# Optimization experiments

Measured on AMD Instinct MI355X. Metric: run time of the kernel, lower is better.

## Reference

```python
import jax, jax.numpy as jnp
import numpy as np

NUM_HEADS = 16
THETA = 10000.0

def _apply_rope(x, positions):
    # x: [B, H, S, dh] with interleaved pairs; positions: [B, S] int
    dh = x.shape[-1]
    inv_freq = THETA ** (-jnp.arange(0, dh, 2, dtype=jnp.float32) / dh)  # [dh/2]
    ang = positions.astype(jnp.float32)[:, None, :, None] * inv_freq  # [B,1,S,dh/2]
    cos, sin = jnp.cos(ang), jnp.sin(ang)
    x1, x2 = x[..., 0::2], x[..., 1::2]
    out_even = x1 * cos - x2 * sin
    out_odd = x1 * sin + x2 * cos
    return jnp.stack([out_even, out_odd], axis=-1).reshape(x.shape)

def setup_inputs() -> dict:
    B, S, D = 2, 2048, 2048
    key = jax.random.key(0)
    ks = jax.random.split(key, 5)
    scale = 0.02
    inp = {
        'in_features': jax.random.normal(ks[0], (B, S, D), dtype=jnp.float32),
        'token_positions': jnp.broadcast_to(jnp.arange(S, dtype=jnp.int32), (B, S)),
        'mask': jnp.tril(jnp.ones((S, S), dtype=bool)),
        'q_proj_weight': jax.random.normal(ks[1], (D, D), dtype=jnp.float32) * scale,
        'k_proj_weight': jax.random.normal(ks[2], (D, D), dtype=jnp.float32) * scale,
        'v_proj_weight': jax.random.normal(ks[3], (D, D), dtype=jnp.float32) * scale,
        'o_proj_weight': jax.random.normal(ks[4], (D, D), dtype=jnp.float32) * scale,
    }
    return inp

def reference(in_features, token_positions, mask, q_proj_weight, k_proj_weight, v_proj_weight, o_proj_weight):
    B, S, d_in = in_features.shape
    d_k = q_proj_weight.shape[0]
    d_v = v_proj_weight.shape[0]
    H = NUM_HEADS
    dk_head, dv_head = d_k // H, d_v // H
    Q = jnp.einsum('bsd,kd->bsk', in_features, q_proj_weight).reshape(B, S, H, dk_head).transpose(0, 2, 1, 3)
    K = jnp.einsum('bsd,kd->bsk', in_features, k_proj_weight).reshape(B, S, H, dk_head).transpose(0, 2, 1, 3)
    V = jnp.einsum('bsd,vd->bsv', in_features, v_proj_weight).reshape(B, S, H, dv_head).transpose(0, 2, 1, 3)
    Q = _apply_rope(Q, token_positions)
    K = _apply_rope(K, token_positions)
    scores = jnp.einsum('bhqd,bhkd->bhqk', Q, K) / jnp.sqrt(jnp.float32(dk_head))
    scores = jnp.where(mask[None, None, :, :], scores, jnp.finfo(scores.dtype).min)
    attn = jax.nn.softmax(scores, axis=-1)
    out = jnp.einsum('bhqk,bhkd->bhqd', attn, V)  # [B,H,S,dv_head]
    out = out.transpose(0, 2, 1, 3).reshape(B, S, d_v)
    return jnp.einsum('bsv,mv->bsm', out, o_proj_weight)
```

## Files before the change

kernel.cpp:

```cpp
#include <hip/hip_runtime.h>
#include <hip/hip_bf16.h>
#include <cstdint>

typedef __bf16 bf16_t;
typedef __bf16 bf16x8 __attribute__((ext_vector_type(8)));
typedef __bf16 bf16x4 __attribute__((ext_vector_type(4)));
typedef float  f32x4  __attribute__((ext_vector_type(4)));

#define B_  2
#define S_  2048
#define D_  2048
#define H_  16
#define DH_ 128
#define LDQ 6144

__device__ __forceinline__ void gload_lds16(const bf16_t* g, bf16_t* l) {
    __builtin_amdgcn_global_load_lds(
        (const __attribute__((address_space(1))) void*)g,
        (__attribute__((address_space(3))) void*)l, 16, 0, 0);
}

__global__ __launch_bounds__(256)
void cast_all_k(const float* __restrict__ X,  const float* __restrict__ Wq,
                const float* __restrict__ Wk, const float* __restrict__ Wv,
                const float* __restrict__ Wo,
                bf16_t* __restrict__ Xb, bf16_t* __restrict__ Wqkv,
                bf16_t* __restrict__ Wob) {
    long bid = blockIdx.x;
    const float* src; bf16_t* dst; long off;
    if      (bid <  8192) { src = X;  dst = Xb;             off = bid;         }
    else if (bid < 12288) { src = Wq; dst = Wqkv;           off = bid - 8192;  }
    else if (bid < 16384) { src = Wk; dst = Wqkv + 4194304; off = bid - 12288; }
    else if (bid < 20480) { src = Wv; dst = Wqkv + 8388608; off = bid - 16384; }
    else                  { src = Wo; dst = Wob;            off = bid - 20480; }
    long i = (off * 256 + threadIdx.x) * 4;
    float4 v = *(const float4*)(src + i);
    bf16x4 o = {(bf16_t)v.x, (bf16_t)v.y, (bf16_t)v.z, (bf16_t)v.w};
    *(bf16x4*)(dst + i) = o;
}

template<bool C_BF16>
__global__ __launch_bounds__(256)
void gemm_nt(const bf16_t* __restrict__ A, int lda,
             const bf16_t* __restrict__ B, int ldb,
             void* __restrict__ Cp, int ldc, int K) {
    __shared__ bf16_t As[128 * 32];
    __shared__ bf16_t Bs[128 * 32];
    const int tid  = threadIdx.x;
    const int wave = tid >> 6;
    const int lane = tid & 63;

    const int ntx = gridDim.x;
    const int nwg = ntx * gridDim.y;
    const int lin = blockIdx.y * ntx + blockIdx.x;
    const int swz = (lin & 7) * (nwg >> 3) + (lin >> 3);
    const long bm = (long)(swz / ntx) * 128;
    const long bn = (long)(swz % ntx) * 128;

    const int srow0 = wave * 16 + (lane >> 2);
    const int srow1 = (4 + wave) * 16 + (lane >> 2);
    const int scol  = (lane & 3) * 8;
    const bf16_t* Ag0 = A + (bm + srow0) * (long)lda + scol;
    const bf16_t* Ag1 = A + (bm + srow1) * (long)lda + scol;
    const bf16_t* Bg0 = B + (bn + srow0) * (long)ldb + scol;
    const bf16_t* Bg1 = B + (bn + srow1) * (long)ldb + scol;
    bf16_t* Al0 = &As[wave * 512];
    bf16_t* Al1 = &As[(4 + wave) * 512];
    bf16_t* Bl0 = &Bs[wave * 512];
    bf16_t* Bl1 = &Bs[(4 + wave) * 512];

    const int wr = (wave >> 1) * 64;
    const int wc = (wave & 1) * 64;
    const int fr = lane & 15;
    const int ko = (lane >> 4) * 8;

    f32x4 acc[4][4] = {};

    for (int k0 = 0; k0 < K; k0 += 32) {
        gload_lds16(Ag0 + k0, Al0);
        gload_lds16(Ag1 + k0, Al1);
        gload_lds16(Bg0 + k0, Bl0);
        gload_lds16(Bg1 + k0, Bl1);
        __syncthreads();
        bf16x8 a[4], b[4];
#pragma unroll
        for (int i = 0; i < 4; ++i)
            a[i] = *(const bf16x8*)&As[(wr + i * 16 + fr) * 32 + ko];
#pragma unroll
        for (int j = 0; j < 4; ++j)
            b[j] = *(const bf16x8*)&Bs[(wc + j * 16 + fr) * 32 + ko];
#pragma unroll
        for (int i = 0; i < 4; ++i)
#pragma unroll
            for (int j = 0; j < 4; ++j)
                acc[i][j] = __builtin_amdgcn_mfma_f32_16x16x32_bf16(a[i], b[j], acc[i][j], 0, 0, 0);
        __syncthreads();
    }

#pragma unroll
    for (int i = 0; i < 4; ++i) {
        long r0 = bm + wr + i * 16 + (lane >> 4) * 4;
#pragma unroll
        for (int j = 0; j < 4; ++j) {
            long cc = bn + wc + j * 16 + (lane & 15);
#pragma unroll
            for (int v = 0; v < 4; ++v) {
                if (C_BF16)
                    ((bf16_t*)Cp)[(r0 + v) * (long)ldc + cc] = (bf16_t)acc[i][j][v];
                else
                    ((float*)Cp)[(r0 + v) * (long)ldc + cc] = acc[i][j][v];
            }
        }
    }
}

__global__ __launch_bounds__(256)
void rope_qk_k(bf16_t* __restrict__ QKV, const int* __restrict__ pos) {
    int t = blockIdx.x * 256 + threadIdx.x;
    int g = t & 15;
    int h = (t >> 4) & 15;
    int s = (t >> 8) & 2047;
    int b = t >> 19;
    long qa = ((long)(b * S_ + s)) * LDQ + h * DH_ + g * 8;
    long ka = qa + D_;
    float p = (float)pos[b * S_ + s];
    bf16x8 q = *(bf16x8*)(QKV + qa);
    bf16x8 k = *(bf16x8*)(QKV + ka);
#pragma unroll
    for (int e = 0; e < 4; ++e) {
        int i = g * 4 + e;
        float invf = exp2f(-(float)i * 0.20762050593045702f);
        float ang = p * invf;
        float sn, cs;
        __sincosf(ang, &sn, &cs);
        float q1 = (float)q[2 * e], q2 = (float)q[2 * e + 1];
        q[2 * e]     = (bf16_t)(q1 * cs - q2 * sn);
        q[2 * e + 1] = (bf16_t)(q1 * sn + q2 * cs);
        float k1 = (float)k[2 * e], k2 = (float)k[2 * e + 1];
        k[2 * e]     = (bf16_t)(k1 * cs - k2 * sn);
        k[2 * e + 1] = (bf16_t)(k1 * sn + k2 * cs);
    }
    *(bf16x8*)(QKV + qa) = q;
    *(bf16x8*)(QKV + ka) = k;
}

__global__ __launch_bounds__(256)
void transpose_v_k(const bf16_t* __restrict__ QKV, bf16_t* __restrict__ Vt) {
    __shared__ bf16_t tile[64][80];
    int t = threadIdx.x;
    int bh = blockIdx.z;
    int b = bh >> 4, h = bh & 15;
    long s0 = (long)blockIdx.x * 64;
    int d0 = blockIdx.y * 64;
    const bf16_t* src = QKV + ((long)b * S_ + s0) * LDQ + 2 * D_ + h * DH_ + d0;
#pragma unroll
    for (int p = 0; p < 2; ++p) {
        int r = (t >> 3) + p * 32;
        int c = (t & 7) * 8;
        *(bf16x8*)&tile[r][c] = *(const bf16x8*)&src[(long)r * LDQ + c];
    }
    __syncthreads();
    bf16_t* dst = Vt + ((long)bh * DH_ + d0) * S_ + s0;
#pragma unroll
    for (int p = 0; p < 2; ++p) {
        int d = (t >> 3) + p * 32;
        int c = (t & 7) * 8;
        bf16x8 v;
#pragma unroll
        for (int e = 0; e < 8; ++e) v[e] = tile[c + e][d];
        *(bf16x8*)&dst[(long)d * S_ + c] = v;
    }
}

__device__ __forceinline__ bf16x8 ldsw(const bf16_t* p, int row, int ecol) {
    return *(const bf16x8*)(p + row * 128 + (ecol ^ ((row & 7) << 3)));
}

__global__ __launch_bounds__(512, 1)
void flash_attn_k(const bf16_t* __restrict__ QKV, const bf16_t* __restrict__ Vt,
                  bf16_t* __restrict__ O) {
    __shared__ bf16_t Ksh[2][128 * 128];
    __shared__ bf16_t Vsh[2][128 * 128];
    __shared__ bf16_t Psh[128 * 128];

    const int tid  = threadIdx.x;
    const int w    = tid >> 6;
    const int lane = tid & 63;
    const int fr   = lane & 15;
    const int hi   = lane >> 4;
    const int hi8  = hi * 8;
    const int hi4  = hi * 4;
    const int w16  = w * 16;

    const int bid = blockIdx.x;
    const int qi  = 15 - (bid >> 5);
    const int bh  = bid & 31;
    const int b   = bh >> 4;
    const int h   = bh & 15;
    const long bS   = (long)b * S_;
    const int  qoff = h * DH_;
    const int  koff = D_ + h * DH_;
    const long vbase = (long)bh * DH_;

#pragma unroll
    for (int p = 0; p < 4; ++p) {
        int idx = p * 512 + tid;
        int row = idx >> 4;
        int sl  = (idx & 15) ^ (row & 7);
        gload_lds16(QKV + (bS + qi * 128 + row) * (long)LDQ + qoff + sl * 8,
                    &Psh[(p * 512 + w * 64) * 8]);
    }
#pragma unroll
    for (int p = 0; p < 4; ++p) {
        int idx = p * 512 + tid;
        int row = idx >> 4;
        int sl  = (idx & 15) ^ (row & 7);
        gload_lds16(QKV + (bS + row) * (long)LDQ + koff + sl * 8,
                    &Ksh[0][(p * 512 + w * 64) * 8]);
        gload_lds16(Vt + (vbase + row) * S_ + sl * 8,
                    &Vsh[0][(p * 512 + w * 64) * 8]);
    }
    asm volatile("s_waitcnt vmcnt(8)" ::: "memory");
    __builtin_amdgcn_s_barrier();
    asm volatile("" ::: "memory");

    bf16x8 qfrag[4];
#pragma unroll
    for (int kk = 0; kk < 4; ++kk)
        qfrag[kk] = ldsw(Psh, w16 + fr, kk * 32 + hi8);

    f32x4 o[8] = {};
    float m_run[4] = {-3.0e38f, -3.0e38f, -3.0e38f, -3.0e38f};
    float l_run[4] = {};

    const float SC = 0.08838834764831845f * 1.4426950408889634f;

    for (int kt = 0; kt <= qi; ++kt) {
        const int buf = kt & 1;
        if (kt < qi) {
#pragma unroll
            for (int p = 0; p < 4; ++p) {
                int idx = p * 512 + tid;
                int row = idx >> 4;
                int sl  = (idx & 15) ^ (row & 7);
                gload_lds16(QKV + (bS + (kt + 1) * 128 + row) * (long)LDQ + koff + sl * 8,
                            &Ksh[buf ^ 1][(p * 512 + w * 64) * 8]);
                gload_lds16(Vt + (vbase + row) * S_ + (kt + 1) * 128 + sl * 8,
                            &Vsh[buf ^ 1][(p * 512 + w * 64) * 8]);
            }
            asm volatile("s_waitcnt vmcnt(8)" ::: "memory");
        } else {
            asm volatile("s_waitcnt vmcnt(0)" ::: "memory");
        }
        __builtin_amdgcn_s_barrier();
        asm volatile("" ::: "memory");

        f32x4 sc[8];
#pragma unroll
        for (int j = 0; j < 8; ++j) {
            f32x4 z = {};
#pragma unroll
            for (int kk = 0; kk < 4; ++kk)
                z = __builtin_amdgcn_mfma_f32_16x16x32_bf16(
                        qfrag[kk], ldsw(Ksh[buf], j * 16 + fr, kk * 32 + hi8), z, 0, 0, 0);
            sc[j] = z;
        }

        const bool diag = (kt == qi);
#pragma unroll
        for (int j = 0; j < 8; ++j)
#pragma unroll
            for (int v = 0; v < 4; ++v) {
                float x = sc[j][v] * SC;
                if (diag && (j * 16 + fr > w16 + hi4 + v)) x = -3.0e38f;
                sc[j][v] = x;
            }

        float fsc[4];
#pragma unroll
        for (int v = 0; v < 4; ++v) {
            float m = fmaxf(fmaxf(fmaxf(sc[0][v], sc[1][v]), fmaxf(sc[2][v], sc[3][v])),
                            fmaxf(fmaxf(sc[4][v], sc[5][v]), fmaxf(sc[6][v], sc[7][v])));
            m = fmaxf(m, __shfl_xor(m, 1));
            m = fmaxf(m, __shfl_xor(m, 2));
            m = fmaxf(m, __shfl_xor(m, 4));
            m = fmaxf(m, __shfl_xor(m, 8));
            float mn = fmaxf(m_run[v], m);
            fsc[v] = exp2f(m_run[v] - mn);
            m_run[v] = mn;
            l_run[v] *= fsc[v];
        }
#pragma unroll
        for (int j2 = 0; j2 < 8; ++j2)
#pragma unroll
            for (int v = 0; v < 4; ++v) o[j2][v] *= fsc[v];

#pragma unroll
        for (int j = 0; j < 8; ++j)
#pragma unroll
            for (int v = 0; v < 4; ++v) {
                float p = exp2f(sc[j][v] - m_run[v]);
                l_run[v] += p;
                int row = w16 + hi4 + v;
                int col = j * 16 + fr;
                Psh[row * 128 + (col ^ ((row & 7) << 3))] = (bf16_t)p;
            }

        asm volatile("s_waitcnt lgkmcnt(0)" ::: "memory");
        __builtin_amdgcn_sched_barrier(0);

        bf16x8 pa[4];
#pragma unroll
        for (int kk = 0; kk < 4; ++kk)
            pa[kk] = ldsw(Psh, w16 + fr, kk * 32 + hi8);
#pragma unroll
        for (int j2 = 0; j2 < 8; ++j2)
#pragma unroll
            for (int kk = 0; kk < 4; ++kk)
                o[j2] = __builtin_amdgcn_mfma_f32_16x16x32_bf16(
                            pa[kk], ldsw(Vsh[buf], j2 * 16 + fr, kk * 32 + hi8), o[j2], 0, 0, 0);

        asm volatile("" ::: "memory");
        __builtin_amdgcn_s_barrier();
        asm volatile("" ::: "memory");
    }

#pragma unroll
    for (int v = 0; v < 4; ++v) {
        float l = l_run[v];
        l += __shfl_xor(l, 1);
        l += __shfl_xor(l, 2);
        l += __shfl_xor(l, 4);
        l += __shfl_xor(l, 8);
        l_run[v] = 1.0f / l;
    }
    const long orow = bS + qi * 128 + w16 + hi4;
#pragma unroll
    for (int j2 = 0; j2 < 8; ++j2)
#pragma unroll
        for (int v = 0; v < 4; ++v)
            O[(orow + v) * D_ + qoff + j2 * 16 + fr] = (bf16_t)(o[j2][v] * l_run[v]);
}

extern "C" void kernel_launch(void* const* d_in, const int* in_sizes, int n_in,
                              void* d_out, int out_size, void* d_ws, size_t ws_size,
                              hipStream_t stream) {
    const float* in_features = (const float*)d_in[0];
    const int*   positions   = (const int*)d_in[1];
    const float* Wq = (const float*)d_in[3];
    const float* Wk = (const float*)d_in[4];
    const float* Wv = (const float*)d_in[5];
    const float* Wo = (const float*)d_in[6];
    float* out = (float*)d_out;

    const size_t SZ_X   = (size_t)B_ * S_ * D_ * 2;
    const size_t SZ_W   = (size_t)D_ * D_ * 2;
    const size_t SZ_QKV = (size_t)B_ * S_ * LDQ * 2;
    if (ws_size < SZ_X * 3 + SZ_W * 4 + SZ_QKV) return;

    char* w = (char*)d_ws;
    bf16_t* Xb      = (bf16_t*)w;   w += SZ_X;
    bf16_t* Wqkv    = (bf16_t*)w;   w += SZ_W * 3;
    bf16_t* Wob     = (bf16_t*)w;   w += SZ_W;
    bf16_t* QKV     = (bf16_t*)w;   w += SZ_QKV;
    bf16_t* Vt      = (bf16_t*)w;   w += SZ_X;
    bf16_t* AttnOut = (bf16_t*)w;   w += SZ_X;

    cast_all_k<<<24576, 256, 0, stream>>>(in_features, Wq, Wk, Wv, Wo, Xb, Wqkv, Wob);

    gemm_nt<true><<<dim3(48, 32), 256, 0, stream>>>(Xb, D_, Wqkv, D_, QKV, LDQ, D_);

    rope_qk_k<<<4096, 256, 0, stream>>>(QKV, positions);
    transpose_v_k<<<dim3(32, 2, 32), 256, 0, stream>>>(QKV, Vt);

    flash_attn_k<<<512, 512, 0, stream>>>(QKV, Vt, AttnOut);

    gemm_nt<false><<<dim3(16, 32), 256, 0, stream>>>(AttnOut, D_, Wob, D_, out, D_, D_);
}
```

Measured before the change: 439.0 us.

## Replace GEMM with 256x256 double-buffered 8-wave kernel using swizzled LDS

Swaps the 128x128, K=32, single-buffer GEMM for a 256x256 tile, K=64 kernel with 8 waves, double-buffered LDS and an XOR-swizzled layout to avoid bank conflicts. The next tile's global-to-LDS loads are interleaved between MFMA quadrants, and s_setprio is raised around the math. The aim is to overlap memory with compute and increase reuse per workgroup. The cost is fewer workgroups (128 for the output projection, below the CU count) and heavy register and LDS use at one block per CU.

New measurement: 425.9 us. -3.0%, faster.

```diff
diff --git a/kernel.cpp b/kernel.cpp
--- a/kernel.cpp
+++ b/kernel.cpp
@@ -19,6 +19,11 @@
         (const __attribute__((address_space(1))) void*)g,
         (__attribute__((address_space(3))) void*)l, 16, 0, 0);
 }
+
+#define BAR  do { asm volatile("" ::: "memory"); __builtin_amdgcn_s_barrier(); \
+                  asm volatile("" ::: "memory"); } while (0)
+#define WAITLGKM do { asm volatile("s_waitcnt lgkmcnt(0)" ::: "memory"); \
+                      __builtin_amdgcn_sched_barrier(0); } while (0)
 
 __global__ __launch_bounds__(256)
 void cast_all_k(const float* __restrict__ X,  const float* __restrict__ Wq,
@@ -39,76 +44,133 @@
     *(bf16x4*)(dst + i) = o;
 }
 
+#define LDS8(s, row, chunk) \
+    (*(const bf16x8*)((s) + (row) * 64 + ((((chunk) ^ ((row) & 7))) << 3)))
+
+#define MMQ(mh, nh, bfx) \
+    _Pragma("unroll") for (int mi = 0; mi < 4; ++mi) { \
+      _Pragma("unroll") for (int ni = 0; ni < 2; ++ni) { \
+        _Pragma("unroll") for (int ks = 0; ks < 2; ++ks) \
+          acc[(mh)*4+mi][(nh)*2+ni] = __builtin_amdgcn_mfma_f32_16x16x32_bf16( \
+              af[mi][ks], bfx[ni][ks], acc[(mh)*4+mi][(nh)*2+ni], 0, 0, 0); } }
+
+__device__ __forceinline__ void ktile8(
+    const bf16_t* sAc, const bf16_t* sBc,
+    bf16_t* sAn, bf16_t* sBn,
+    bool do_stage, long k0s,
+    const bf16_t* Agp, const bf16_t* Bgp, int lda, int ldb,
+    int wm, int wn, int fr, int hi, int w,
+    f32x4 acc[8][4]) {
+    bf16x8 af[4][2], bf0[2][2], bf1[2][2];
+#pragma unroll
+    for (int mi = 0; mi < 4; ++mi)
+#pragma unroll
+        for (int ks = 0; ks < 2; ++ks)
+            af[mi][ks] = LDS8(sAc, wm * 128 + mi * 16 + fr, ks * 4 + hi);
+#pragma unroll
+    for (int ni = 0; ni < 2; ++ni)
+#pragma unroll
+        for (int ks = 0; ks < 2; ++ks)
+            bf0[ni][ks] = LDS8(sBc, wn * 64 + ni * 16 + fr, ks * 4 + hi);
+    if (do_stage) {
+#pragma unroll
+        for (int p = 0; p < 4; ++p)
+            gload_lds16(Agp + (long)(p * 64) * lda + k0s, sAn + p * 4096 + w * 512);
+    }
+    BAR; WAITLGKM;
+    __builtin_amdgcn_s_setprio(1);
+    MMQ(0, 0, bf0);
+    __builtin_amdgcn_s_setprio(0);
+    BAR;
+#pragma unroll
+    for (int ni = 0; ni < 2; ++ni)
+#pragma unroll
+        for (int ks = 0; ks < 2; ++ks)
+            bf1[ni][ks] = LDS8(sBc, wn * 64 + 32 + ni * 16 + fr, ks * 4 + hi);
+    if (do_stage) {
+#pragma unroll
+        for (int p = 0; p < 4; ++p)
+            gload_lds16(Bgp + (long)(p * 64) * ldb + k0s, sBn + p * 4096 + w * 512);
+    }
+    BAR; WAITLGKM;
+    __builtin_amdgcn_s_setprio(1);
+    MMQ(0, 1, bf1);
+    __builtin_amdgcn_s_setprio(0);
+    BAR;
+#pragma unroll
+    for (int mi = 0; mi < 4; ++mi)
+#pragma unroll
+        for (int ks = 0; ks < 2; ++ks)
+            af[mi][ks] = LDS8(sAc, wm * 128 + 64 + mi * 16 + fr, ks * 4 + hi);
+    BAR; WAITLGKM;
+    __builtin_amdgcn_s_setprio(1);
+    MMQ(1, 0, bf0);
+    __builtin_amdgcn_s_setprio(0);
+    BAR;
+    __builtin_amdgcn_s_setprio(1);
+    MMQ(1, 1, bf1);
+    __builtin_amdgcn_s_setprio(0);
+    if (do_stage) asm volatile("s_waitcnt vmcnt(0)" ::: "memory");
+    BAR;
+}
+
 template<bool C_BF16>
-__global__ __launch_bounds__(256)
-void gemm_nt(const bf16_t* __restrict__ A, int lda,
-             const bf16_t* __restrict__ B, int ldb,
-             void* __restrict__ Cp, int ldc, int K) {
-    __shared__ bf16_t As[128 * 32];
-    __shared__ bf16_t Bs[128 * 32];
+__global__ __launch_bounds__(512, 1)
+void gemm_nt8(const bf16_t* __restrict__ A, int lda,
+              const bf16_t* __restrict__ B, int ldb,
+              void* __restrict__ Cp, int ldc, int K, int nbx) {
+    __shared__ bf16_t sA[2][256 * 64];
+    __shared__ bf16_t sB[2][256 * 64];
     const int tid  = threadIdx.x;
-    const int wave = tid >> 6;
+    const int w    = tid >> 6;
     const int lane = tid & 63;
-
-    const int ntx = gridDim.x;
-    const int nwg = ntx * gridDim.y;
-    const int lin = blockIdx.y * ntx + blockIdx.x;
+    const int fr   = lane & 15;
+    const int hi   = lane >> 4;
+    const int wm   = w >> 2;
+    const int wn   = w & 3;
+
+    const int nwg = gridDim.x;
+    const int lin = blockIdx.x;
     const int swz = (lin & 7) * (nwg >> 3) + (lin >> 3);
-    const long bm = (long)(swz / ntx) * 128;
-    const long bn = (long)(swz % ntx) * 128;
-
-    const int srow0 = wave * 16 + (lane >> 2);
-    const int srow1 = (4 + wave) * 16 + (lane >> 2);
-    const int scol  = (lane & 3) * 8;
-    const bf16_t* Ag0 = A + (bm + srow0) * (long)lda + scol;
-    const bf16_t* Ag1 = A + (bm + srow1) * (long)lda + scol;
-    const bf16_t* Bg0 = B + (bn + srow0) * (long)ldb + scol;
-    const bf16_t* Bg1 = B + (bn + srow1) * (long)ldb + scol;
-    bf16_t* Al0 = &As[wave * 512];
-    bf16_t* Al1 = &As[(4 + wave) * 512];
-    bf16_t* Bl0 = &Bs[wave * 512];
-    bf16_t* Bl1 = &Bs[(4 + wave) * 512];
-
-    const int wr = (wave >> 1) * 64;
-    const int wc = (wave & 1) * 64;
-    const int fr = lane & 15;
-    const int ko = (lane >> 4) * 8;
-
-    f32x4 acc[4][4] = {};
-
-    for (int k0 = 0; k0 < K; k0 += 32) {
-        gload_lds16(Ag0 + k0, Al0);
-        gload_lds16(Ag1 + k0, Al1);
-        gload_lds16(Bg0 + k0, Bl0);
-        gload_lds16(Bg1 + k0, Bl1);
-        __syncthreads();
-        bf16x8 a[4], b[4];
-#pragma unroll
-        for (int i = 0; i < 4; ++i)
-            a[i] = *(const bf16x8*)&As[(wr + i * 16 + fr) * 32 + ko];
-#pragma unroll
-        for (int j = 0; j < 4; ++j)
-            b[j] = *(const bf16x8*)&Bs[(wc + j * 16 + fr) * 32 + ko];
-#pragma unroll
-        for (int i = 0; i < 4; ++i)
-#pragma unroll
-            for (int j = 0; j < 4; ++j)
-                acc[i][j] = __builtin_amdgcn_mfma_f32_16x16x32_bf16(a[i], b[j], acc[i][j], 0, 0, 0);
-        __syncthreads();
-    }
-
-#pragma unroll
-    for (int i = 0; i < 4; ++i) {
-        long r0 = bm + wr + i * 16 + (lane >> 4) * 4;
-#pragma unroll
-        for (int j = 0; j < 4; ++j) {
-            long cc = bn + wc + j * 16 + (lane & 15);
+    const long bm = (long)(swz / nbx) * 256;
+    const long bn = (long)(swz % nbx) * 256;
+
+    const int  srow = tid >> 3;
+    const int  scol = ((tid & 7) ^ (srow & 7)) * 8;
+    const bf16_t* Agp = A + (bm + srow) * (long)lda + scol;
+    const bf16_t* Bgp = B + (bn + srow) * (long)ldb + scol;
+
+    f32x4 acc[8][4] = {};
+    const int nkt = K >> 6;
+
+#pragma unroll
+    for (int p = 0; p < 4; ++p)
+        gload_lds16(Agp + (long)(p * 64) * lda, sA[0] + p * 4096 + w * 512);
+#pragma unroll
+    for (int p = 0; p < 4; ++p)
+        gload_lds16(Bgp + (long)(p * 64) * ldb, sB[0] + p * 4096 + w * 512);
+    asm volatile("s_waitcnt vmcnt(0)" ::: "memory");
+    BAR;
+
+    for (int kt = 0; kt < nkt; kt += 2) {
+        ktile8(sA[0], sB[0], sA[1], sB[1], true, (long)(kt + 1) << 6,
+               Agp, Bgp, lda, ldb, wm, wn, fr, hi, w, acc);
+        ktile8(sA[1], sB[1], sA[0], sB[0], (kt + 2) < nkt, (long)(kt + 2) << 6,
+               Agp, Bgp, lda, ldb, wm, wn, fr, hi, w, acc);
+    }
+
+#pragma unroll
+    for (int m = 0; m < 8; ++m) {
+        long r0 = bm + wm * 128 + m * 16 + hi * 4;
+#pragma unroll
+        for (int n = 0; n < 4; ++n) {
+            long cc = bn + wn * 64 + n * 16 + fr;
 #pragma unroll
             for (int v = 0; v < 4; ++v) {
                 if (C_BF16)
-                    ((bf16_t*)Cp)[(r0 + v) * (long)ldc + cc] = (bf16_t)acc[i][j][v];
+                    ((bf16_t*)Cp)[(r0 + v) * (long)ldc + cc] = (bf16_t)acc[m][n][v];
                 else
-                    ((float*)Cp)[(r0 + v) * (long)ldc + cc] = acc[i][j][v];
+                    ((float*)Cp)[(r0 + v) * (long)ldc + cc] = acc[m][n][v];
             }
         }
     }
@@ -368,12 +430,12 @@
 
     cast_all_k<<<24576, 256, 0, stream>>>(in_features, Wq, Wk, Wv, Wo, Xb, Wqkv, Wob);
 
-    gemm_nt<true><<<dim3(48, 32), 256, 0, stream>>>(Xb, D_, Wqkv, D_, QKV, LDQ, D_);
+    gemm_nt8<true><<<384, 512, 0, stream>>>(Xb, D_, Wqkv, D_, QKV, LDQ, D_, 24);
 
     rope_qk_k<<<4096, 256, 0, stream>>>(QKV, positions);
     transpose_v_k<<<dim3(32, 2, 32), 256, 0, stream>>>(QKV, Vt);
 
     flash_attn_k<<<512, 512, 0, stream>>>(QKV, Vt, AttnOut);
 
-    gemm_nt<false><<<dim3(16, 32), 256, 0, stream>>>(AttnOut, D_, Wob, D_, out, D_, D_);
-}
+    gemm_nt8<false><<<128, 512, 0, stream>>>(AttnOut, D_, Wob, D_, out, D_, D_, 8);
+}
```
